# Performance work log

Measured on AMD Instinct MI355X. Metric: run time of the kernel, lower is better.

## Reference

```python
import jax, jax.numpy as jnp
import numpy as np

NUM_HEADS = 8


def setup_inputs() -> dict:
    key = jax.random.key(0)
    k1, k2, k3 = jax.random.split(key, 3)
    B, N, C = 4, 8448, 512
    x = jax.random.normal(k1, (B, N, C), dtype=jnp.float32)
    w_qkv = jax.random.normal(k2, (3 * C, C), dtype=jnp.float32) * (C ** -0.5)
    w_proj = jax.random.normal(k3, (C, C), dtype=jnp.float32) * (C ** -0.5)
    b_proj = jnp.zeros((C,), dtype=jnp.float32)
    return {"x": x, "w_qkv": w_qkv, "w_proj": w_proj, "b_proj": b_proj, "N_points": 8192}


def reference(x, w_qkv, w_proj, b_proj, N_points):
    B, N, C = x.shape
    H = NUM_HEADS
    hd = C // H
    scale = hd ** -0.5
    N_latent = N - N_points

    qkv = (x @ w_qkv.T).reshape(B, N, 3, H, hd).transpose(2, 0, 3, 1, 4)  # [3,B,H,N,hd]
    q, k, v = qkv[0], qkv[1], qkv[2]
    q_l, k_l, v_l = q[:, :, :N_latent], k[:, :, :N_latent], v[:, :, :N_latent]
    q_p, k_p, v_p = q[:, :, N_latent:], k[:, :, N_latent:], v[:, :, N_latent:]

    # joint cross+self attention for the points
    attn_cross = jnp.einsum('bhpd,bhld->bhpl', q_p, k_l) * scale        # [B,H,P,L]
    attn_self = jnp.sum(q_p * k_p, axis=-1, keepdims=True) * scale      # [B,H,P,1]
    attn_joint = jax.nn.softmax(jnp.concatenate([attn_cross, attn_self], axis=-1), axis=-1)

    sum_cross = jnp.einsum('bhpl,bhld->bhpd', attn_joint[..., :N_latent], v_l)
    sum_self = attn_joint[..., N_latent:] * v_p
    out_points = (sum_cross + sum_self).transpose(0, 2, 1, 3).reshape(B, N_points, C)

    # standard self-attention over latent tokens
    attn_latent = jax.nn.softmax(jnp.einsum('bhqd,bhkd->bhqk', q_l, k_l) * scale, axis=-1)
    out_latent = jnp.einsum('bhqk,bhkd->bhqd', attn_latent, v_l).transpose(0, 2, 1, 3).reshape(B, N_latent, C)

    output = jnp.concatenate([out_latent, out_points], axis=1) @ w_proj.T + b_proj
    attn_mean = attn_joint[..., :-1].mean(axis=1)  # [B,P,L]
    return output, attn_mean
```

## Files before the change

### kernel.cpp

```cpp
#include <hip/hip_runtime.h>

#define BQ 4
#define NH 8
#define NTOK 8448
#define NLAT 256
#define NPTS 8192
#define CDIM 512
#define HD 64
#define SCALE 0.125f
#define L2E 1.4426950408889634f
#define SC2 0.1803368801111204f

typedef __attribute__((ext_vector_type(8))) short short8b;
typedef __attribute__((ext_vector_type(4))) float f32x4;

static __device__ __forceinline__ float4 ld4(const float* p) { return *(const float4*)p; }

static __device__ __forceinline__ short f2b(float f) {
  union { float f; unsigned u; } c; c.f = f;
  unsigned u = c.u;
  u += ((u >> 16) & 1u) + 0x7fffu;
  return (short)(u >> 16);
}

static __device__ __forceinline__ float b2f(unsigned short u) {
  union { unsigned u; float f; } c; c.u = ((unsigned)u) << 16; return c.f;
}

static __device__ __forceinline__ int cvtpk(float lo, float hi) {
  int r; asm("v_cvt_pk_bf16_f32 %0, %1, %2" : "=v"(r) : "v"(lo), "v"(hi)); return r;
}

static __device__ __forceinline__ float fexp2(float x) {
  float r; asm("v_exp_f32 %0, %1" : "=v"(r) : "v"(x)); return r;
}

static __device__ __forceinline__ void gload_lds16(const unsigned short* g, unsigned short* l) {
  __builtin_amdgcn_global_load_lds((const __attribute__((address_space(1))) void*)g,
                                   (__attribute__((address_space(3))) void*)l, 16, 0, 0);
}

__global__ __launch_bounds__(256) void to_bf16_3(const float* __restrict__ a, unsigned short* __restrict__ ao_, int na8,
                                                 const float* __restrict__ b, unsigned short* __restrict__ bo, int nb8,
                                                 const float* __restrict__ c, unsigned short* __restrict__ co, int nc8) {
  int i = blockIdx.x * 256 + threadIdx.x;
  const float* src; unsigned short* dst; int idx;
  if (i < na8) { src = a; dst = ao_; idx = i; }
  else if (i < na8 + nb8) { src = b; dst = bo; idx = i - na8; }
  else if (i < na8 + nb8 + nc8) { src = c; dst = co; idx = i - na8 - nb8; }
  else return;
  float4 x0 = ld4(src + (size_t)idx * 8);
  float4 x1 = ld4(src + (size_t)idx * 8 + 4);
  short8b r;
  r[0] = f2b(x0.x); r[1] = f2b(x0.y); r[2] = f2b(x0.z); r[3] = f2b(x0.w);
  r[4] = f2b(x1.x); r[5] = f2b(x1.y); r[6] = f2b(x1.z); r[7] = f2b(x1.w);
  *(short8b*)&dst[(size_t)idx * 8] = r;
}

#define STAGE128(PA, PB, kt, s)                                                              \
  do {                                                                                       \
    const int _c = (kt) * 64 + scell;                                                        \
    unsigned short* _d = &lds[(s) * 16384 + t * 8];                                          \
    gload_lds16((PA) + (size_t)(m0 + sr) * CDIM + _c,       _d);                             \
    gload_lds16((PA) + (size_t)(m0 + 32 + sr) * CDIM + _c,  _d + 2048);                      \
    gload_lds16((PA) + (size_t)(m0 + 64 + sr) * CDIM + _c,  _d + 4096);                      \
    gload_lds16((PA) + (size_t)(m0 + 96 + sr) * CDIM + _c,  _d + 6144);                      \
    gload_lds16((PB) + (size_t)(j0 + sr) * CDIM + _c,       _d + 8192);                      \
    gload_lds16((PB) + (size_t)(j0 + 32 + sr) * CDIM + _c,  _d + 10240);                     \
    gload_lds16((PB) + (size_t)(j0 + 64 + sr) * CDIM + _c,  _d + 12288);                     \
    gload_lds16((PB) + (size_t)(j0 + 96 + sr) * CDIM + _c,  _d + 14336);                     \
  } while (0)

#define GEMM128_BODY(PA, PB)                                                                 \
  __shared__ unsigned short lds[32768];                                                      \
  const int fl = blockIdx.y * gridDim.x + blockIdx.x;                                        \
  const int nchunk = (gridDim.x * gridDim.y) >> 3;                                           \
  const int wid = (fl & 7) * nchunk + (fl >> 3);                                             \
  const int m0 = (wid / gridDim.x) * 128;                                                    \
  const int j0 = (wid % gridDim.x) * 128;                                                    \
  const int t = threadIdx.x;                                                                 \
  const int lane = t & 63, wave = t >> 6;                                                    \
  const int wr = wave >> 1, wc = wave & 1;                                                   \
  const int lm = lane & 15, lq = lane >> 4;                                                  \
  const int sr = t >> 3;                                                                     \
  const int scell = (((t & 7) ^ (sr & 7)) << 3);                                             \
  f32x4 acc[4][4] = {};                                                                      \
  STAGE128(PA, PB, 0, 0);                                                                    \
  STAGE128(PA, PB, 1, 1);                                                                    \
  for (int kt = 0; kt < 8; ++kt) {                                                           \
    const int s = kt & 1;                                                                    \
    if (kt == 7) asm volatile("s_waitcnt vmcnt(0)" ::: "memory");                            \
    else         asm volatile("s_waitcnt vmcnt(8)" ::: "memory");                            \
    __builtin_amdgcn_s_barrier();                                                            \
    const unsigned short* sb = &lds[s * 16384];                                              \
    short8b af[4][2], bf[4][2];                                                              \
    _Pragma("unroll")                                                                        \
    for (int mt = 0; mt < 4; ++mt) {                                                         \
      const int RA = wr * 64 + mt * 16 + lm;                                                 \
      const int RB = wc * 64 + mt * 16 + lm;                                                 \
      af[mt][0] = *(const short8b*)&sb[RA * 64 + ((lq ^ (RA & 7)) << 3)];                    \
      af[mt][1] = *(const short8b*)&sb[RA * 64 + (((4 | lq) ^ (RA & 7)) << 3)];              \
      bf[mt][0] = *(const short8b*)&sb[8192 + RB * 64 + ((lq ^ (RB & 7)) << 3)];             \
      bf[mt][1] = *(const short8b*)&sb[8192 + RB * 64 + (((4 | lq) ^ (RB & 7)) << 3)];       \
    }                                                                                        \
    __builtin_amdgcn_s_setprio(1);                                                           \
    _Pragma("unroll")                                                                        \
    for (int ks = 0; ks < 2; ++ks)                                                           \
      _Pragma("unroll")                                                                      \
      for (int mt = 0; mt < 4; ++mt)                                                         \
        _Pragma("unroll")                                                                    \
        for (int nt = 0; nt < 4; ++nt)                                                       \
          acc[mt][nt] = __builtin_amdgcn_mfma_f32_16x16x32_bf16(af[mt][ks], bf[nt][ks],      \
                                                                acc[mt][nt], 0, 0, 0);       \
    __builtin_amdgcn_s_setprio(0);                                                           \
    asm volatile("s_waitcnt lgkmcnt(0)" ::: "memory");                                       \
    __builtin_amdgcn_s_barrier();                                                            \
    __builtin_amdgcn_sched_barrier(0);                                                       \
    if (kt < 6) STAGE128(PA, PB, kt + 2, s);                                                 \
  }

__global__ __launch_bounds__(256, 2) void qkv_mfma(const unsigned short* __restrict__ xb,
                                                   const unsigned short* __restrict__ wb,
                                                   unsigned short* __restrict__ qo,
                                                   unsigned short* __restrict__ ko,
                                                   unsigned short* __restrict__ vo) {
  GEMM128_BODY(xb, wb)
  const int s_ = j0 >> 9;
  unsigned short* dst = (s_ == 0) ? qo : ((s_ == 1) ? ko : vo);
  const int b = m0 / NTOK;
  const int n0 = m0 % NTOK;
  const int h = ((j0 >> 6) + wc) & 7;
#pragma unroll
  for (int mt = 0; mt < 4; ++mt) {
#pragma unroll
    for (int r = 0; r < 4; ++r) {
      const int n = n0 + wr * 64 + mt * 16 + lq * 4 + r;
      const size_t ob = (((size_t)b * NH + h) * NTOK + n) * HD;
#pragma unroll
      for (int nt = 0; nt < 4; ++nt)
        dst[ob + nt * 16 + lm] = (unsigned short)f2b(acc[mt][nt][r]);
    }
  }
}

__global__ __launch_bounds__(256, 2) void proj_mfma(const unsigned short* __restrict__ ab,
                                                    const unsigned short* __restrict__ wpb,
                                                    const float* __restrict__ bias,
                                                    float* __restrict__ out) {
  GEMM128_BODY(ab, wpb)
#pragma unroll
  for (int mt = 0; mt < 4; ++mt) {
#pragma unroll
    for (int r = 0; r < 4; ++r) {
      const int m = m0 + wr * 64 + mt * 16 + lq * 4 + r;
#pragma unroll
      for (int nt = 0; nt < 4; ++nt) {
        const int j = j0 + wc * 64 + nt * 16 + lm;
        out[(size_t)m * CDIM + j] = acc[mt][nt][r] + bias[j];
      }
    }
  }
}

__global__ __launch_bounds__(512, 2) void attn_pm(const unsigned short* __restrict__ qb,
                                                  const unsigned short* __restrict__ kb,
                                                  const unsigned short* __restrict__ vb,
                                                  unsigned short* __restrict__ aob,
                                                  float* __restrict__ out1) {
  __shared__ unsigned short kl[2][16384];
  __shared__ unsigned short vt[2][16384];
  const int t = threadIdx.x;
  const int lane = t & 63, wave = t >> 6;
  const int lm = lane & 15, lq = lane >> 4;
  if (blockIdx.x < 64) {
    const int idx = blockIdx.x;
    const int bh = idx >> 1, half = idx & 1;
    const size_t bhb = (size_t)bh * NTOK * HD;
    {
      const int vr = t >> 1, dh = t & 1;
      const unsigned short* vg = vb + bhb + (size_t)vr * HD + dh * 32;
      short8b rv[4];
#pragma unroll
      for (int i = 0; i < 4; ++i) rv[i] = *(const short8b*)(vg + i * 8);
      const int gsw = vr >> 3, wi = vr & 7;
#pragma unroll
      for (int i = 0; i < 4; ++i) {
        const int d0 = dh * 4 + i;
#pragma unroll
        for (int j = 0; j < 8; ++j)
          vt[0][(d0 * 8 + j) * 256 + ((gsw ^ j) << 3) + wi] = (unsigned short)rv[i][j];
      }
    }
    __syncthreads();
    const int b = bh >> 3, h = bh & 7;
    const int q0 = half * 128 + wave * 16;
    const size_t qrow = bhb + (size_t)(q0 + lm) * HD;
    const short8b bq0 = *(const short8b*)(qb + qrow + lq * 8);
    const short8b bq1 = *(const short8b*)(qb + qrow + 32 + lq * 8);
    f32x4 s[16] = {};
    __builtin_amdgcn_s_setprio(1);
#pragma unroll
    for (int mt = 0; mt < 16; ++mt) {
      const int krow = ((mt >> 1) << 5) + ((lm >> 2) << 3) + ((mt & 1) << 2) + (lm & 3);
      const unsigned short* kr = kb + bhb + (size_t)krow * HD + lq * 8;
      s[mt] = __builtin_amdgcn_mfma_f32_16x16x32_bf16(*(const short8b*)kr, bq0, s[mt], 0, 0, 0);
      s[mt] = __builtin_amdgcn_mfma_f32_16x16x32_bf16(*(const short8b*)(kr + 32), bq1, s[mt], 0, 0, 0);
    }
    __builtin_amdgcn_s_setprio(0);
    float mx = -1e30f;
#pragma unroll
    for (int mt = 0; mt < 16; ++mt)
#pragma unroll
      for (int r = 0; r < 4; ++r) mx = fmaxf(mx, s[mt][r]);
    mx = fmaxf(mx, __shfl_xor(mx, 16));
    mx = fmaxf(mx, __shfl_xor(mx, 32));
    const float m2 = mx * SCALE * L2E;
    float sum = 0.f;
#pragma unroll
    for (int mt = 0; mt < 16; ++mt)
#pragma unroll
      for (int r = 0; r < 4; ++r) {
        float e = fexp2(fmaf(s[mt][r], SC2, -m2));
        s[mt][r] = e;
        sum += e;
      }
    sum += __shfl_xor(sum, 16);
    sum += __shfl_xor(sum, 32);
    const float inv = 1.f / sum;
#pragma unroll
    for (int mt = 0; mt < 16; ++mt)
#pragma unroll
      for (int r = 0; r < 4; ++r) s[mt][r] *= inv;
    f32x4 o[4] = {};
    __builtin_amdgcn_s_setprio(1);
#pragma unroll
    for (int ks = 0; ks < 8; ++ks) {
      union { int i[4]; short8b v; } af;
      af.i[0] = cvtpk(s[2 * ks][0], s[2 * ks][1]);
      af.i[1] = cvtpk(s[2 * ks][2], s[2 * ks][3]);
      af.i[2] = cvtpk(s[2 * ks + 1][0], s[2 * ks + 1][1]);
      af.i[3] = cvtpk(s[2 * ks + 1][2], s[2 * ks + 1][3]);
#pragma unroll
      for (int ntd = 0; ntd < 4; ++ntd) {
        const int row = ntd * 16 + lm;
        const short8b bv = *(const short8b*)&vt[0][row * 256 + ((((ks << 2) | lq) ^ (lm & 7)) << 3)];
        o[ntd] = __builtin_amdgcn_mfma_f32_16x16x32_bf16(af.v, bv, o[ntd], 0, 0, 0);
      }
    }
    __builtin_amdgcn_s_setprio(0);
#pragma unroll
    for (int ntd = 0; ntd < 4; ++ntd)
#pragma unroll
      for (int r = 0; r < 4; ++r) {
        const int n = q0 + lq * 4 + r;
        aob[((size_t)b * NTOK + n) * CDIM + h * HD + ntd * 16 + lm] =
            (unsigned short)f2b(o[ntd][r]);
      }
    return;
  }
  const int bidx = blockIdx.x - 64;
  const int b = bidx >> 6, pq = bidx & 63;
  const int pp0 = pq * 128 + wave * 16;
  const size_t bb = (size_t)(b * NH) * NTOK * HD;
  const int vr = t >> 1, dh = t & 1;
  const int gsw = vr >> 3, wi = vr & 7;
  short8b vregs[4];
#define ISSUE_K(hh, sl_)                                                          \
  do {                                                                            \
    const unsigned short* kg = kb + bb + (size_t)(hh) * NTOK * HD;                \
    _Pragma("unroll")                                                             \
    for (int c = 0; c < 4; ++c) {                                                 \
      const int rr = c * 64 + (t >> 3);                                           \
      const int mt_ = rr >> 4, w_ = rr & 15;                                      \
      const int g = 32 * (mt_ >> 1) + 8 * (w_ >> 2) + 4 * (mt_ & 1) + (w_ & 3);   \
      gload_lds16(kg + g * HD + (((t & 7) ^ (rr & 7)) << 3),                      \
                  &kl[sl_][(c * 512 + t) * 8]);                                   \
    }                                                                             \
  } while (0)
#define READ_V(hh)                                                                \
  do {                                                                            \
    const unsigned short* vg = vb + bb + (size_t)(hh) * NTOK * HD +               \
                               (size_t)vr * HD + dh * 32;                         \
    _Pragma("unroll")                                                             \
    for (int i = 0; i < 4; ++i) vregs[i] = *(const short8b*)(vg + i * 8);         \
  } while (0)
#define WRITE_V(sl_)                                                              \
  do {                                                                            \
    _Pragma("unroll")                                                             \
    for (int i = 0; i < 4; ++i) {                                                 \
      const int d0 = dh * 4 + i;                                                  \
      _Pragma("unroll")                                                           \
      for (int j = 0; j < 8; ++j)                                                 \
        vt[sl_][(d0 * 8 + j) * 256 + ((gsw ^ j) << 3) + wi] =                     \
            (unsigned short)vregs[i][j];                                          \
    }                                                                             \
  } while (0)
  f32x4 prob[16] = {};
  ISSUE_K(0, 0); READ_V(0);
  asm volatile("s_waitcnt vmcnt(0)" ::: "memory");
  WRITE_V(0);
  ISSUE_K(1, 1); READ_V(1);
  __syncthreads();
  for (int h = 0; h < NH; ++h) {
    const int sl = h & 1;
    const size_t hb = bb + (size_t)h * NTOK * HD;
    const size_t qrow = hb + (size_t)(NLAT + pp0 + lm) * HD;
    const short8b bq0 = *(const short8b*)(qb + qrow + lq * 8);
    const short8b bq1 = *(const short8b*)(qb + qrow + 32 + lq * 8);
    f32x4 s[16] = {};
    __builtin_amdgcn_s_setprio(1);
#pragma unroll
    for (int mt = 0; mt < 16; ++mt) {
      const int rr = mt * 16 + lm;
      const short8b ak0 = *(const short8b*)&kl[sl][rr * 64 + ((lq ^ (rr & 7)) << 3)];
      const short8b ak1 = *(const short8b*)&kl[sl][rr * 64 + (((4 | lq) ^ (rr & 7)) << 3)];
      s[mt] = __builtin_amdgcn_mfma_f32_16x16x32_bf16(ak0, bq0, s[mt], 0, 0, 0);
      s[mt] = __builtin_amdgcn_mfma_f32_16x16x32_bf16(ak1, bq1, s[mt], 0, 0, 0);
    }
    __builtin_amdgcn_s_setprio(0);
    float sself = 0.f;
    {
      const unsigned short* qp = qb + qrow + lq * 16;
      const unsigned short* kp = kb + qrow + lq * 16;
      short8b q0 = *(const short8b*)qp, q1 = *(const short8b*)(qp + 8);
      short8b k0 = *(const short8b*)kp, k1 = *(const short8b*)(kp + 8);
#pragma unroll
      for (int j = 0; j < 8; ++j)
        sself += b2f((unsigned short)q0[j]) * b2f((unsigned short)k0[j]) +
                 b2f((unsigned short)q1[j]) * b2f((unsigned short)k1[j]);
    }
    sself += __shfl_xor(sself, 16);
    sself += __shfl_xor(sself, 32);
    sself *= SCALE;
    float mx = -1e30f;
#pragma unroll
    for (int mt = 0; mt < 16; ++mt)
#pragma unroll
      for (int r = 0; r < 4; ++r) mx = fmaxf(mx, s[mt][r]);
    mx = fmaxf(mx, __shfl_xor(mx, 16));
    mx = fmaxf(mx, __shfl_xor(mx, 32));
    const float m = fmaxf(mx * SCALE, sself);
    const float m2 = m * L2E;
    float sum = 0.f;
#pragma unroll
    for (int mt = 0; mt < 16; ++mt)
#pragma unroll
      for (int r = 0; r < 4; ++r) {
        float e = fexp2(fmaf(s[mt][r], SC2, -m2));
        s[mt][r] = e;
        sum += e;
      }
    sum += __shfl_xor(sum, 16);
    sum += __shfl_xor(sum, 32);
    const float pself = fexp2(fmaf(sself, L2E, -m2));
    const float inv = 1.f / (sum + pself);
#pragma unroll
    for (int mt = 0; mt < 16; ++mt)
#pragma unroll
      for (int r = 0; r < 4; ++r) {
        const float pn = s[mt][r] * inv;
        s[mt][r] = pn;
        prob[mt][r] += pn;
      }
    f32x4 o[4] = {};
    __builtin_amdgcn_s_setprio(1);
#pragma unroll
    for (int ks = 0; ks < 8; ++ks) {
      union { int i[4]; short8b v; } af;
      af.i[0] = cvtpk(s[2 * ks][0], s[2 * ks][1]);
      af.i[1] = cvtpk(s[2 * ks][2], s[2 * ks][3]);
      af.i[2] = cvtpk(s[2 * ks + 1][0], s[2 * ks + 1][1]);
      af.i[3] = cvtpk(s[2 * ks + 1][2], s[2 * ks + 1][3]);
#pragma unroll
      for (int ntd = 0; ntd < 4; ++ntd) {
        const int row = ntd * 16 + lm;
        const short8b bv = *(const short8b*)&vt[sl][row * 256 + ((((ks << 2) | lq) ^ (lm & 7)) << 3)];
        o[ntd] = __builtin_amdgcn_mfma_f32_16x16x32_bf16(af.v, bv, o[ntd], 0, 0, 0);
      }
    }
    __builtin_amdgcn_s_setprio(0);
    const float pisl = pself * inv;
    float psl[4];
#pragma unroll
    for (int r = 0; r < 4; ++r) psl[r] = __shfl(pisl, lq * 4 + r);
#pragma unroll
    for (int ntd = 0; ntd < 4; ++ntd)
#pragma unroll
      for (int r = 0; r < 4; ++r) {
        const int n = NLAT + pp0 + lq * 4 + r;
        const float v_ = b2f(vb[hb + (size_t)n * HD + ntd * 16 + lm]);
        aob[((size_t)b * NTOK + n) * CDIM + h * HD + ntd * 16 + lm] =
            (unsigned short)f2b(o[ntd][r] + psl[r] * v_);
      }
    __syncthreads();
    if (h < 7) {
      asm volatile("s_waitcnt vmcnt(0)" ::: "memory");
      WRITE_V(sl ^ 1);
      if (h < 6) { ISSUE_K(h + 2, sl); READ_V(h + 2); }
      __syncthreads();
    }
  }
  const size_t orow = ((size_t)b * NPTS + pp0 + lm) * NLAT;
#pragma unroll
  for (int mt = 0; mt < 16; ++mt) {
    const int col = 32 * (mt >> 1) + 8 * lq + 4 * (mt & 1);
    *(float4*)&out1[orow + col] = make_float4(prob[mt][0] * 0.125f, prob[mt][1] * 0.125f,
                                              prob[mt][2] * 0.125f, prob[mt][3] * 0.125f);
  }
#undef ISSUE_K
#undef READ_V
#undef WRITE_V
}

extern "C" void kernel_launch(void* const* d_in, const int* in_sizes, int n_in,
                              void* d_out, int out_size, void* d_ws, size_t ws_size,
                              hipStream_t stream) {
  const float* x      = (const float*)d_in[0];
  const float* w_qkv  = (const float*)d_in[1];
  const float* w_proj = (const float*)d_in[2];
  const float* b_proj = (const float*)d_in[3];
  const size_t QSZ = (size_t)BQ * NH * NTOK * HD;
  unsigned short* qb  = (unsigned short*)d_ws;
  unsigned short* kb  = qb + QSZ;
  unsigned short* vb  = kb + QSZ;
  unsigned short* aob = vb + QSZ;
  unsigned short* xb  = aob + QSZ;
  unsigned short* wb  = xb + QSZ;
  unsigned short* wpb = wb + 786432;
  float* out0 = (float*)d_out;
  float* out1 = out0 + (size_t)BQ * NTOK * CDIM;

  to_bf16_3<<<8960, 256, 0, stream>>>(x, xb, 2162688, w_qkv, wb, 98304, w_proj, wpb, 32768);
  qkv_mfma<<<dim3(12, 264), 256, 0, stream>>>(xb, wb, qb, kb, vb);
  attn_pm<<<320, 512, 0, stream>>>(qb, kb, vb, aob, out1);
  proj_mfma<<<dim3(4, 264), 256, 0, stream>>>(aob, wpb, b_proj, out0);
}
```

Before: 181.6 us.

## Split attention key range across two wave halves in 1024-thread blocks

The point-attention kernel moves from 512 to 1024 threads per block. Two groups of eight waves each take half of the 256 latent keys for the same query rows. The partial row max, row sum and PV output are combined through new LDS exchange buffers, with extra barriers. The V tile goes from double to single buffering, and the load work is split so one half issues the K async copies while the other stages V. The aim is more parallelism and shorter per-wave dependency chains, at the cost of extra synchronisation, LDS traffic and a launch bound that may squeeze registers.

```diff
diff --git a/kernel.cpp b/kernel.cpp
--- a/kernel.cpp
+++ b/kernel.cpp
@@ -162,13 +162,16 @@
   }
 }
 
-__global__ __launch_bounds__(512, 2) void attn_pm(const unsigned short* __restrict__ qb,
-                                                  const unsigned short* __restrict__ kb,
-                                                  const unsigned short* __restrict__ vb,
-                                                  unsigned short* __restrict__ aob,
-                                                  float* __restrict__ out1) {
+__global__ __launch_bounds__(1024, 4) void attn_pm(const unsigned short* __restrict__ qb,
+                                                   const unsigned short* __restrict__ kb,
+                                                   const unsigned short* __restrict__ vb,
+                                                   unsigned short* __restrict__ aob,
+                                                   float* __restrict__ out1) {
   __shared__ unsigned short kl[2][16384];
-  __shared__ unsigned short vt[2][16384];
+  __shared__ unsigned short vt[16384];
+  __shared__ float xch_o[8][64][17];
+  __shared__ float xch_m[8][2][16];
+  __shared__ float xch_s[8][2][16];
   const int t = threadIdx.x;
   const int lane = t & 63, wave = t >> 6;
   const int lm = lane & 15, lq = lane >> 4;
@@ -176,7 +179,7 @@
     const int idx = blockIdx.x;
     const int bh = idx >> 1, half = idx & 1;
     const size_t bhb = (size_t)bh * NTOK * HD;
-    {
+    if (t < 512) {
       const int vr = t >> 1, dh = t & 1;
       const unsigned short* vg = vb + bhb + (size_t)vr * HD + dh * 32;
       short8b rv[4];
@@ -188,10 +191,11 @@
         const int d0 = dh * 4 + i;
 #pragma unroll
         for (int j = 0; j < 8; ++j)
-          vt[0][(d0 * 8 + j) * 256 + ((gsw ^ j) << 3) + wi] = (unsigned short)rv[i][j];
+          vt[(d0 * 8 + j) * 256 + ((gsw ^ j) << 3) + wi] = (unsigned short)rv[i][j];
       }
     }
     __syncthreads();
+    if (t >= 512) return;
     const int b = bh >> 3, h = bh & 7;
     const int q0 = half * 128 + wave * 16;
     const size_t qrow = bhb + (size_t)(q0 + lm) * HD;
@@ -243,7 +247,7 @@
 #pragma unroll
       for (int ntd = 0; ntd < 4; ++ntd) {
         const int row = ntd * 16 + lm;
-        const short8b bv = *(const short8b*)&vt[0][row * 256 + ((((ks << 2) | lq) ^ (lm & 7)) << 3)];
+        const short8b bv = *(const short8b*)&vt[row * 256 + ((((ks << 2) | lq) ^ (lm & 7)) << 3)];
         o[ntd] = __builtin_amdgcn_mfma_f32_16x16x32_bf16(af.v, bv, o[ntd], 0, 0, 0);
       }
     }
@@ -260,9 +264,12 @@
   }
   const int bidx = blockIdx.x - 64;
   const int b = bidx >> 6, pq = bidx & 63;
-  const int pp0 = pq * 128 + wave * 16;
+  const int hf = wave >> 3, pr = wave & 7;
+  const int pp0 = pq * 128 + pr * 16;
+  const int mtbase = hf * 8;
   const size_t bb = (size_t)(b * NH) * NTOK * HD;
-  const int vr = t >> 1, dh = t & 1;
+  const int tt = t - 512;
+  const int vr = tt >> 1, dh = tt & 1;
   const int gsw = vr >> 3, wi = vr & 7;
   short8b vregs[4];
 #define ISSUE_K(hh, sl_)                                                          \
@@ -284,22 +291,21 @@
     _Pragma("unroll")                                                             \
     for (int i = 0; i < 4; ++i) vregs[i] = *(const short8b*)(vg + i * 8);         \
   } while (0)
-#define WRITE_V(sl_)                                                              \
+#define WRITE_V()                                                                 \
   do {                                                                            \
     _Pragma("unroll")                                                             \
     for (int i = 0; i < 4; ++i) {                                                 \
       const int d0 = dh * 4 + i;                                                  \
       _Pragma("unroll")                                                           \
       for (int j = 0; j < 8; ++j)                                                 \
-        vt[sl_][(d0 * 8 + j) * 256 + ((gsw ^ j) << 3) + wi] =                     \
-            (unsigned short)vregs[i][j];                                          \
+        vt[(d0 * 8 + j) * 256 + ((gsw ^ j) << 3) + wi] = (unsigned short)vregs[i][j]; \
     }                                                                             \
   } while (0)
-  f32x4 prob[16] = {};
-  ISSUE_K(0, 0); READ_V(0);
+  f32x4 prob[8] = {};
+  if (t < 512) { ISSUE_K(0, 0); ISSUE_K(1, 1); }
+  else READ_V(0);
   asm volatile("s_waitcnt vmcnt(0)" ::: "memory");
-  WRITE_V(0);
-  ISSUE_K(1, 1); READ_V(1);
+  if (t >= 512) { WRITE_V(); READ_V(1); }
   __syncthreads();
   for (int h = 0; h < NH; ++h) {
     const int sl = h & 1;
@@ -307,15 +313,15 @@
     const size_t qrow = hb + (size_t)(NLAT + pp0 + lm) * HD;
     const short8b bq0 = *(const short8b*)(qb + qrow + lq * 8);
     const short8b bq1 = *(const short8b*)(qb + qrow + 32 + lq * 8);
-    f32x4 s[16] = {};
+    f32x4 s[8] = {};
     __builtin_amdgcn_s_setprio(1);
 #pragma unroll
-    for (int mt = 0; mt < 16; ++mt) {
-      const int rr = mt * 16 + lm;
+    for (int mtl = 0; mtl < 8; ++mtl) {
+      const int rr = (mtbase + mtl) * 16 + lm;
       const short8b ak0 = *(const short8b*)&kl[sl][rr * 64 + ((lq ^ (rr & 7)) << 3)];
       const short8b ak1 = *(const short8b*)&kl[sl][rr * 64 + (((4 | lq) ^ (rr & 7)) << 3)];
-      s[mt] = __builtin_amdgcn_mfma_f32_16x16x32_bf16(ak0, bq0, s[mt], 0, 0, 0);
-      s[mt] = __builtin_amdgcn_mfma_f32_16x16x32_bf16(ak1, bq1, s[mt], 0, 0, 0);
+      s[mtl] = __builtin_amdgcn_mfma_f32_16x16x32_bf16(ak0, bq0, s[mtl], 0, 0, 0);
+      s[mtl] = __builtin_amdgcn_mfma_f32_16x16x32_bf16(ak1, bq1, s[mtl], 0, 0, 0);
     }
     __builtin_amdgcn_s_setprio(0);
     float sself = 0.f;
@@ -334,78 +340,96 @@
     sself *= SCALE;
     float mx = -1e30f;
 #pragma unroll
-    for (int mt = 0; mt < 16; ++mt)
-#pragma unroll
-      for (int r = 0; r < 4; ++r) mx = fmaxf(mx, s[mt][r]);
+    for (int mtl = 0; mtl < 8; ++mtl)
+#pragma unroll
+      for (int r = 0; r < 4; ++r) mx = fmaxf(mx, s[mtl][r]);
     mx = fmaxf(mx, __shfl_xor(mx, 16));
     mx = fmaxf(mx, __shfl_xor(mx, 32));
-    const float m = fmaxf(mx * SCALE, sself);
+    if (lane < 16) xch_m[pr][hf][lane] = mx;
+    __syncthreads();
+    const float m = fmaxf(fmaxf(mx, xch_m[pr][hf ^ 1][lm]) * SCALE, sself);
     const float m2 = m * L2E;
     float sum = 0.f;
 #pragma unroll
-    for (int mt = 0; mt < 16; ++mt)
+    for (int mtl = 0; mtl < 8; ++mtl)
 #pragma unroll
       for (int r = 0; r < 4; ++r) {
-        float e = fexp2(fmaf(s[mt][r], SC2, -m2));
-        s[mt][r] = e;
+        float e = fexp2(fmaf(s[mtl][r], SC2, -m2));
+        s[mtl][r] = e;
         sum += e;
       }
     sum += __shfl_xor(sum, 16);
     sum += __shfl_xor(sum, 32);
+    if (lane < 16) xch_s[pr][hf][lane] = sum;
+    __syncthreads();
     const float pself = fexp2(fmaf(sself, L2E, -m2));
-    const float inv = 1.f / (sum + pself);
-#pragma unroll
-    for (int mt = 0; mt < 16; ++mt)
+    const float inv = 1.f / (sum + xch_s[pr][hf ^ 1][lm] + pself);
+#pragma unroll
+    for (int mtl = 0; mtl < 8; ++mtl)
 #pragma unroll
       for (int r = 0; r < 4; ++r) {
-        const float pn = s[mt][r] * inv;
-        s[mt][r] = pn;
-        prob[mt][r] += pn;
+        const float pn = s[mtl][r] * inv;
+        s[mtl][r] = pn;
+        prob[mtl][r] += pn;
       }
     f32x4 o[4] = {};
     __builtin_amdgcn_s_setprio(1);
 #pragma unroll
-    for (int ks = 0; ks < 8; ++ks) {
+    for (int ksl = 0; ksl < 4; ++ksl) {
+      const int gks = hf * 4 + ksl;
       union { int i[4]; short8b v; } af;
-      af.i[0] = cvtpk(s[2 * ks][0], s[2 * ks][1]);
-      af.i[1] = cvtpk(s[2 * ks][2], s[2 * ks][3]);
-      af.i[2] = cvtpk(s[2 * ks + 1][0], s[2 * ks + 1][1]);
-      af.i[3] = cvtpk(s[2 * ks + 1][2], s[2 * ks + 1][3]);
+      af.i[0] = cvtpk(s[2 * ksl][0], s[2 * ksl][1]);
+      af.i[1] = cvtpk(s[2 * ksl][2], s[2 * ksl][3]);
+      af.i[2] = cvtpk(s[2 * ksl + 1][0], s[2 * ksl + 1][1]);
+      af.i[3] = cvtpk(s[2 * ksl + 1][2], s[2 * ksl + 1][3]);
 #pragma unroll
       for (int ntd = 0; ntd < 4; ++ntd) {
         const int row = ntd * 16 + lm;
-        const short8b bv = *(const short8b*)&vt[sl][row * 256 + ((((ks << 2) | lq) ^ (lm & 7)) << 3)];
+        const short8b bv = *(const short8b*)&vt[row * 256 + ((((gks << 2) | lq) ^ (lm & 7)) << 3)];
         o[ntd] = __builtin_amdgcn_mfma_f32_16x16x32_bf16(af.v, bv, o[ntd], 0, 0, 0);
       }
     }
     __builtin_amdgcn_s_setprio(0);
-    const float pisl = pself * inv;
-    float psl[4];
-#pragma unroll
-    for (int r = 0; r < 4; ++r) psl[r] = __shfl(pisl, lq * 4 + r);
-#pragma unroll
-    for (int ntd = 0; ntd < 4; ++ntd)
-#pragma unroll
-      for (int r = 0; r < 4; ++r) {
-        const int n = NLAT + pp0 + lq * 4 + r;
-        const float v_ = b2f(vb[hb + (size_t)n * HD + ntd * 16 + lm]);
-        aob[((size_t)b * NTOK + n) * CDIM + h * HD + ntd * 16 + lm] =
-            (unsigned short)f2b(o[ntd][r] + psl[r] * v_);
-      }
+    if (hf == 1) {
+#pragma unroll
+      for (int ntd = 0; ntd < 4; ++ntd)
+#pragma unroll
+        for (int r = 0; r < 4; ++r) xch_o[pr][lane][ntd * 4 + r] = o[ntd][r];
+    }
     __syncthreads();
+    if (hf == 0) {
+      const float pisl = pself * inv;
+      float psl[4];
+#pragma unroll
+      for (int r = 0; r < 4; ++r) psl[r] = __shfl(pisl, lq * 4 + r);
+#pragma unroll
+      for (int ntd = 0; ntd < 4; ++ntd)
+#pragma unroll
+        for (int r = 0; r < 4; ++r) {
+          const int n = NLAT + pp0 + lq * 4 + r;
+          const float v_ = b2f(vb[hb + (size_t)n * HD + ntd * 16 + lm]);
+          const float tot = o[ntd][r] + xch_o[pr][lane][ntd * 4 + r] + psl[r] * v_;
+          aob[((size_t)b * NTOK + n) * CDIM + h * HD + ntd * 16 + lm] = (unsigned short)f2b(tot);
+        }
+    }
     if (h < 7) {
       asm volatile("s_waitcnt vmcnt(0)" ::: "memory");
-      WRITE_V(sl ^ 1);
-      if (h < 6) { ISSUE_K(h + 2, sl); READ_V(h + 2); }
+      if (t >= 512) {
+        WRITE_V();
+        if (h < 6) READ_V(h + 2);
+      } else if (h < 6) {
+        ISSUE_K(h + 2, sl);
+      }
       __syncthreads();
     }
   }
   const size_t orow = ((size_t)b * NPTS + pp0 + lm) * NLAT;
 #pragma unroll
-  for (int mt = 0; mt < 16; ++mt) {
-    const int col = 32 * (mt >> 1) + 8 * lq + 4 * (mt & 1);
-    *(float4*)&out1[orow + col] = make_float4(prob[mt][0] * 0.125f, prob[mt][1] * 0.125f,
-                                              prob[mt][2] * 0.125f, prob[mt][3] * 0.125f);
+  for (int mtl = 0; mtl < 8; ++mtl) {
+    const int gmt = mtbase + mtl;
+    const int col = 32 * (gmt >> 1) + 8 * lq + 4 * (gmt & 1);
+    *(float4*)&out1[orow + col] = make_float4(prob[mtl][0] * 0.125f, prob[mtl][1] * 0.125f,
+                                              prob[mtl][2] * 0.125f, prob[mtl][3] * 0.125f);
   }
 #undef ISSUE_K
 #undef READ_V
@@ -432,6 +456,6 @@
 
   to_bf16_3<<<8960, 256, 0, stream>>>(x, xb, 2162688, w_qkv, wb, 98304, w_proj, wpb, 32768);
   qkv_mfma<<<dim3(12, 264), 256, 0, stream>>>(xb, wb, qb, kb, vb);
-  attn_pm<<<320, 512, 0, stream>>>(qb, kb, vb, aob, out1);
+  attn_pm<<<320, 1024, 0, stream>>>(qb, kb, vb, aob, out1);
   proj_mfma<<<dim3(4, 264), 256, 0, stream>>>(aob, wpb, b_proj, out0);
 }
```

Result: slower. 237.1 us (+30.6%).
